# Kernel optimization log

Measured on AMD Instinct MI355X. Metric: run time of the kernel, lower is better.

## Reference

```python
import jax, jax.numpy as jnp
import numpy as np

B, N, IN_F, OUT_F, H, NUM_EDGE_TYPES = 16, 512, 256, 256, 8, 50
HEAD_DIM = OUT_F // H
LN_EPS = 1e-5


def setup_inputs() -> dict:
    key = jax.random.key(0)
    ks = jax.random.split(key, 8)
    x = jax.random.normal(ks[0], (B, N, IN_F), dtype=jnp.float32)
    adj = jax.random.randint(ks[1], (B, N, N), 0, 2, dtype=jnp.int32)
    edge_types = jax.random.randint(ks[2], (B, N, N), 0, NUM_EDGE_TYPES, dtype=jnp.int32)
    # Parameters (torch Linear stores weight as [out, in]; we keep [in, out] for x @ W)
    W = jax.random.normal(ks[3], (IN_F, OUT_F), dtype=jnp.float32) / np.sqrt(IN_F)
    a1 = jax.random.normal(ks[4], (HEAD_DIM,), dtype=jnp.float32) / np.sqrt(HEAD_DIM)
    a2 = jax.random.normal(ks[5], (HEAD_DIM,), dtype=jnp.float32) / np.sqrt(HEAD_DIM)
    edge_emb = jax.random.normal(ks[6], (NUM_EDGE_TYPES, H), dtype=jnp.float32) * 0.02
    edge_emb = edge_emb.at[0].set(0.0)  # padding_idx=0
    ln_gamma = jnp.ones((OUT_F,), dtype=jnp.float32)
    ln_beta = jnp.zeros((OUT_F,), dtype=jnp.float32)
    return {"x": x, "adj": adj, "edge_types": edge_types, "W": W, "a1": a1,
            "a2": a2, "edge_emb": edge_emb, "ln_gamma": ln_gamma, "ln_beta": ln_beta}


def reference(x, adj, edge_types, W, a1, a2, edge_emb, ln_gamma, ln_beta):
    Bx, Nx, _ = x.shape
    # Wh: [B, N, H, D]
    Wh = (x @ W).reshape(Bx, Nx, H, HEAD_DIM)
    # per-node attention scalars: [B, N, H]
    s1 = jnp.einsum('bnhd,d->bnh', Wh, a1)
    s2 = jnp.einsum('bnhd,d->bnh', Wh, a2)
    # e: [B, N(i), N(j), H]
    e = s1[:, :, None, :] + s2[:, None, :, :] + edge_emb[edge_types]
    e = jnp.where(e > 0, e, 0.2 * e)  # leaky_relu(0.2)
    e = jnp.where((adj == 0)[..., None], jnp.float32(-1e9), e)
    alpha = jax.nn.softmax(e, axis=2)  # softmax over j
    # (dropout omitted: eval mode / deterministic reference)
    h = jnp.einsum('bijh,bjhd->bihd', alpha, Wh).reshape(Bx, Nx, OUT_F)
    # LayerNorm over last dim
    mu = jnp.mean(h, axis=-1, keepdims=True)
    var = jnp.mean(jnp.square(h - mu), axis=-1, keepdims=True)
    hn = (h - mu) * jax.lax.rsqrt(var + LN_EPS) * ln_gamma + ln_beta
    return jax.nn.elu(hn)
```

## Files before the change

kernel.cpp:

```cpp
#include <hip/hip_runtime.h>
#include <hip/hip_bf16.h>
#include <stdint.h>

namespace gat {
constexpr int NB   = 16;
constexpr int NN   = 512;
constexpr int FIN  = 256;
constexpr int FOUT = 256;
constexpr int H    = 8;
constexpr int NE   = 50;
constexpr float L2E  = 1.4426950408889634f;
constexpr float MASK = -115.41500f;
}
using namespace gat;

typedef __attribute__((ext_vector_type(8))) short short8;
typedef __attribute__((ext_vector_type(4))) float f32x4;

__device__ __forceinline__ unsigned pk_bf16(unsigned ulo, unsigned uhi) {
  return __builtin_amdgcn_perm(uhi, ulo, 0x07060302u);
}
__device__ __forceinline__ unsigned pk2f(float a, float b) {
  return pk_bf16(__float_as_uint(a) + 0x8000u, __float_as_uint(b) + 0x8000u);
}

__global__ __launch_bounds__(256) void k_prep(const float* __restrict__ Wm,
                                              unsigned short* __restrict__ WbT) {
  const int k = blockIdx.x;
  const int f = threadIdx.x;
  const unsigned u = __float_as_uint(Wm[k * FOUT + f]) + 0x8000u;
  WbT[f * FIN + k] = (unsigned short)(u >> 16);
}

__global__ __launch_bounds__(256) void k_pack(const int* __restrict__ adj,
                                              const int* __restrict__ ety,
                                              unsigned* __restrict__ codes) {
  const size_t base = ((size_t)blockIdx.x * 256 + threadIdx.x) * 16;
  const int4* ap = (const int4*)(adj + base);
  const int4* ep = (const int4*)(ety + base);
  unsigned o[4];
  #pragma unroll
  for (int g = 0; g < 4; ++g) {
    const int4 a = ap[g];
    const int4 e = ep[g];
    o[g] = (unsigned)(e.x | (a.x << 6))
         | ((unsigned)(e.y | (a.y << 6)) << 8)
         | ((unsigned)(e.z | (a.z << 6)) << 16)
         | ((unsigned)(e.w | (a.w << 6)) << 24);
  }
  uint4 v; v.x = o[0]; v.y = o[1]; v.z = o[2]; v.w = o[3];
  *(uint4*)(codes + base / 4) = v;
}

__global__ __launch_bounds__(512, 4) void k_gemm(
    const float* __restrict__ x, const unsigned short* __restrict__ WbT,
    const float* __restrict__ a1, const float* __restrict__ a2,
    unsigned short* __restrict__ WhT, float* __restrict__ s1, float* __restrict__ s2T)
{
  __shared__ alignas(16) unsigned short xS[16 * 264];
  __shared__ float redG[256 * 18];
  const int t    = threadIdx.x;
  const int row0 = blockIdx.x * 16;

  {
    const int r  = t >> 5;
    const int kb = (t & 31) * 8;
    const float4* xg = (const float4*)(x + (size_t)(row0 + r) * FIN + kb);
    const float4 v0 = xg[0], v1 = xg[1];
    uint4 o;
    o.x = pk2f(v0.x, v0.y); o.y = pk2f(v0.z, v0.w);
    o.z = pk2f(v1.x, v1.y); o.w = pk2f(v1.z, v1.w);
    *(uint4*)&xS[r * 264 + kb] = o;
  }
  __syncthreads();

  const int W    = t >> 6;
  const int w    = W & 3;
  const int kh   = W >> 2;
  const int L    = t & 63;
  const int nn   = L & 15;
  const int quad = L >> 4;
  const unsigned short* wb = WbT + (size_t)(w * 64 + nn) * FIN + kh * 128 + quad * 8;
  const unsigned short* xp = &xS[nn * 264 + kh * 128 + quad * 8];

  f32x4 acc0 = {0.f,0.f,0.f,0.f}, acc1 = {0.f,0.f,0.f,0.f};
  f32x4 acc2 = {0.f,0.f,0.f,0.f}, acc3 = {0.f,0.f,0.f,0.f};

  #pragma unroll
  for (int kc = 0; kc < 4; ++kc) {
    const int k0 = kc * 32;
    const short8 A  = *(const short8*)(xp + k0);
    const short8 B0 = *(const short8*)(wb + k0);
    const short8 B1 = *(const short8*)(wb + 16 * FIN + k0);
    const short8 B2 = *(const short8*)(wb + 32 * FIN + k0);
    const short8 B3 = *(const short8*)(wb + 48 * FIN + k0);
    acc0 = __builtin_amdgcn_mfma_f32_16x16x32_bf16(A, B0, acc0, 0, 0, 0);
    acc1 = __builtin_amdgcn_mfma_f32_16x16x32_bf16(A, B1, acc1, 0, 0, 0);
    acc2 = __builtin_amdgcn_mfma_f32_16x16x32_bf16(A, B2, acc2, 0, 0, 0);
    acc3 = __builtin_amdgcn_mfma_f32_16x16x32_bf16(A, B3, acc3, 0, 0, 0);
  }

  const int tt = (w << 6) | L;
  if (kh == 1) {
    float* rp = redG + tt * 18;
    rp[0]=acc0[0]; rp[1]=acc0[1]; rp[2]=acc0[2]; rp[3]=acc0[3];
    rp[4]=acc1[0]; rp[5]=acc1[1]; rp[6]=acc1[2]; rp[7]=acc1[3];
    rp[8]=acc2[0]; rp[9]=acc2[1]; rp[10]=acc2[2]; rp[11]=acc2[3];
    rp[12]=acc3[0]; rp[13]=acc3[1]; rp[14]=acc3[2]; rp[15]=acc3[3];
  }
  __syncthreads();
  if (kh == 1) return;

  {
    const float* rp = redG + tt * 18;
    acc0[0]+=rp[0]; acc0[1]+=rp[1]; acc0[2]+=rp[2]; acc0[3]+=rp[3];
    acc1[0]+=rp[4]; acc1[1]+=rp[5]; acc1[2]+=rp[6]; acc1[3]+=rp[7];
    acc2[0]+=rp[8]; acc2[1]+=rp[9]; acc2[2]+=rp[10]; acc2[3]+=rp[11];
    acc3[0]+=rp[12]; acc3[1]+=rp[13]; acc3[2]+=rp[14]; acc3[3]+=rp[15];
  }

  const int b     = row0 >> 9;
  const int node0 = (row0 & 511) + quad * 4;
  f32x4 accs[4] = {acc0, acc1, acc2, acc3};

  #pragma unroll
  for (int ft = 0; ft < 4; ++ft) {
    const int f = w * 64 + ft * 16 + nn;
    uint2 o;
    o.x = pk2f(accs[ft][0], accs[ft][1]);
    o.y = pk2f(accs[ft][2], accs[ft][3]);
    *(uint2*)(WhT + (size_t)((b * 8 + (f >> 5)) * 32 + (f & 31)) * 512 + node0) = o;
  }

  const float a1lo = a1[nn], a1hi = a1[16 + nn];
  const float a2lo = a2[nn], a2hi = a2[16 + nn];
  #pragma unroll
  for (int hh = 0; hh < 2; ++hh) {
    const int h = w * 2 + hh;
    const f32x4 e0 = accs[hh * 2], e1 = accs[hh * 2 + 1];
    float p1[4], p2[4];
    #pragma unroll
    for (int r = 0; r < 4; ++r) {
      p1[r] = e0[r] * a1lo + e1[r] * a1hi;
      p2[r] = e0[r] * a2lo + e1[r] * a2hi;
    }
    #pragma unroll
    for (int r = 0; r < 4; ++r) {
      p1[r] += __shfl_xor(p1[r], 1); p2[r] += __shfl_xor(p2[r], 1);
      p1[r] += __shfl_xor(p1[r], 2); p2[r] += __shfl_xor(p2[r], 2);
      p1[r] += __shfl_xor(p1[r], 4); p2[r] += __shfl_xor(p2[r], 4);
      p1[r] += __shfl_xor(p1[r], 8); p2[r] += __shfl_xor(p2[r], 8);
    }
    if (nn == 0) {
      float4 sv; sv.x = p2[0] * L2E; sv.y = p2[1] * L2E; sv.z = p2[2] * L2E; sv.w = p2[3] * L2E;
      *(float4*)(s2T + (size_t)(b * 8 + h) * 512 + node0) = sv;
      #pragma unroll
      for (int r = 0; r < 4; ++r)
        s1[(size_t)(row0 + quad * 4 + r) * H + h] = p1[r] * L2E;
    }
  }
}

__global__ __launch_bounds__(512, 4) void k_attn(
    const unsigned char* __restrict__ codes,
    const float* __restrict__ s1, const float* __restrict__ s2T,
    const unsigned short* __restrict__ WhT, const float* __restrict__ emb,
    const float* __restrict__ gam, const float* __restrict__ bet,
    float* __restrict__ out)
{
  __shared__ float2 embS[4 * 64];
  __shared__ float2 lnS[16 * 4];
  __shared__ float  s2S[8 * 512];
  __shared__ float  redS[256 * 18];

  const int t    = threadIdx.x;
  const int b    = blockIdx.x >> 5;
  const int i0   = (blockIdx.x & 31) * 16;
  const int W    = t >> 6;
  const int w    = W & 3;
  const int jh   = W >> 2;
  const int L    = t & 63;
  const int i    = L & 15;
  const int quad = L >> 4;
  const int h0   = w, h1 = w + 4;

  {
    const float4* sg = (const float4*)(s2T + (size_t)b * 8 * 512);
    float4* ss = (float4*)s2S;
    ss[t]       = sg[t];
    ss[t + 512] = sg[t + 512];
  }
  if (t < 256) {
    const int wp = t >> 6, e = t & 63;
    if (e < NE) {
      float2 v; v.x = emb[e * H + wp] * L2E; v.y = emb[e * H + wp + 4] * L2E;
      embS[t] = v;
    }
  }

  const int row   = b * NN + i0 + i;
  const int jbase = jh * 256;

  uint2 cw[8];
  {
    const unsigned char* cp = codes + (size_t)row * NN + jbase + quad * 8;
    #pragma unroll
    for (int kc = 0; kc < 8; ++kc) cw[kc] = *(const uint2*)(cp + kc * 32);
  }

  const float si0 = s1[(size_t)row * H + h0];
  const float si1 = s1[(size_t)row * H + h1];
  const unsigned short* wt00 = WhT + (size_t)((b * 8 + h0) * 32 + i)      * 512;
  const unsigned short* wt01 = WhT + (size_t)((b * 8 + h0) * 32 + 16 + i) * 512;
  const unsigned short* wt10 = WhT + (size_t)((b * 8 + h1) * 32 + i)      * 512;
  const unsigned short* wt11 = WhT + (size_t)((b * 8 + h1) * 32 + 16 + i) * 512;

  f32x4 acc00 = {0.f,0.f,0.f,0.f}, acc01 = {0.f,0.f,0.f,0.f};
  f32x4 acc10 = {0.f,0.f,0.f,0.f}, acc11 = {0.f,0.f,0.f,0.f};
  float l0 = 0.f, l1 = 0.f;

  __syncthreads();

  #pragma unroll 2
  for (int kc = 0; kc < 8; ++kc) {
    const int ja = jbase + kc * 32 + quad * 8;
    const short8 A00 = *(const short8*)(wt00 + ja);
    const short8 A01 = *(const short8*)(wt01 + ja);
    const short8 A10 = *(const short8*)(wt10 + ja);
    const short8 A11 = *(const short8*)(wt11 + ja);
    const float4 sa0 = *(const float4*)&s2S[h0 * 512 + ja];
    const float4 sb0 = *(const float4*)&s2S[h0 * 512 + ja + 4];
    const float4 sa1 = *(const float4*)&s2S[h1 * 512 + ja];
    const float4 sb1 = *(const float4*)&s2S[h1 * 512 + ja + 4];

    const float s20[8] = {sa0.x, sa0.y, sa0.z, sa0.w, sb0.x, sb0.y, sb0.z, sb0.w};
    const float s21[8] = {sa1.x, sa1.y, sa1.z, sa1.w, sb1.x, sb1.y, sb1.z, sb1.w};

    unsigned u0[8], u1[8];
    #pragma unroll
    for (int q = 0; q < 8; ++q) {
      const unsigned cword = (q < 4) ? cw[kc].x : cw[kc].y;
      const unsigned c = (cword >> ((q & 3) * 8)) & 0x7fu;
      const bool on = c >= 64u;
      const float2 em = embS[w * 64 + (c & 63u)];
      float e0 = si0 + s20[q] + em.x;
      float e1 = si1 + s21[q] + em.y;
      e0 = fmaxf(e0, 0.2f * e0);
      e1 = fmaxf(e1, 0.2f * e1);
      e0 = on ? e0 : MASK;
      e1 = on ? e1 : MASK;
      const float p0 = exp2f(e0);
      const float p1 = exp2f(e1);
      l0 += p0; l1 += p1;
      u0[q] = __float_as_uint(p0) + 0x8000u;
      u1[q] = __float_as_uint(p1) + 0x8000u;
    }
    uint4 U0, U1;
    U0.x = pk_bf16(u0[0], u0[1]); U0.y = pk_bf16(u0[2], u0[3]);
    U0.z = pk_bf16(u0[4], u0[5]); U0.w = pk_bf16(u0[6], u0[7]);
    U1.x = pk_bf16(u1[0], u1[1]); U1.y = pk_bf16(u1[2], u1[3]);
    U1.z = pk_bf16(u1[4], u1[5]); U1.w = pk_bf16(u1[6], u1[7]);
    const short8 B0 = __builtin_bit_cast(short8, U0);
    const short8 B1 = __builtin_bit_cast(short8, U1);

    acc00 = __builtin_amdgcn_mfma_f32_16x16x32_bf16(A00, B0, acc00, 0, 0, 0);
    acc01 = __builtin_amdgcn_mfma_f32_16x16x32_bf16(A01, B0, acc01, 0, 0, 0);
    acc10 = __builtin_amdgcn_mfma_f32_16x16x32_bf16(A10, B1, acc10, 0, 0, 0);
    acc11 = __builtin_amdgcn_mfma_f32_16x16x32_bf16(A11, B1, acc11, 0, 0, 0);
  }

  l0 += __shfl_xor(l0, 16); l0 += __shfl_xor(l0, 32);
  l1 += __shfl_xor(l1, 16); l1 += __shfl_xor(l1, 32);

  const int tt = (w << 6) | L;
  if (jh == 1) {
    float* rp = redS + tt * 18;
    rp[0]=acc00[0]; rp[1]=acc00[1]; rp[2]=acc00[2]; rp[3]=acc00[3];
    rp[4]=acc01[0]; rp[5]=acc01[1]; rp[6]=acc01[2]; rp[7]=acc01[3];
    rp[8]=acc10[0]; rp[9]=acc10[1]; rp[10]=acc10[2]; rp[11]=acc10[3];
    rp[12]=acc11[0]; rp[13]=acc11[1]; rp[14]=acc11[2]; rp[15]=acc11[3];
    rp[16]=l0; rp[17]=l1;
  }
  __syncthreads();

  float vals[16]; float mu, rstd;
  if (jh == 0) {
    const float* rp = redS + tt * 18;
    acc00[0]+=rp[0]; acc00[1]+=rp[1]; acc00[2]+=rp[2]; acc00[3]+=rp[3];
    acc01[0]+=rp[4]; acc01[1]+=rp[5]; acc01[2]+=rp[6]; acc01[3]+=rp[7];
    acc10[0]+=rp[8]; acc10[1]+=rp[9]; acc10[2]+=rp[10]; acc10[3]+=rp[11];
    acc11[0]+=rp[12]; acc11[1]+=rp[13]; acc11[2]+=rp[14]; acc11[3]+=rp[15];
    l0 += rp[16]; l1 += rp[17];
    const float inv0 = __builtin_amdgcn_rcpf(l0);
    const float inv1 = __builtin_amdgcn_rcpf(l1);
    #pragma unroll
    for (int r = 0; r < 4; ++r) {
      vals[r]      = acc00[r] * inv0;
      vals[4 + r]  = acc01[r] * inv0;
      vals[8 + r]  = acc10[r] * inv1;
      vals[12 + r] = acc11[r] * inv1;
    }
    float s = 0.f, ss = 0.f;
    #pragma unroll
    for (int k = 0; k < 16; ++k) { s += vals[k]; ss += vals[k] * vals[k]; }
    s += __shfl_xor(s, 16); ss += __shfl_xor(ss, 16);
    s += __shfl_xor(s, 32); ss += __shfl_xor(ss, 32);
    if (quad == 0) { float2 v; v.x = s; v.y = ss; lnS[i * 4 + w] = v; }
  }
  __syncthreads();
  if (jh == 1) return;

  {
    float S = 0.f, SS = 0.f;
    #pragma unroll
    for (int ww = 0; ww < 4; ++ww) { const float2 v = lnS[i * 4 + ww]; S += v.x; SS += v.y; }
    mu = S * (1.0f / 256.0f);
    const float var = SS * (1.0f / 256.0f) - mu * mu;
    rstd = rsqrtf(var + 1e-5f);
  }

  const int fb[4] = { h0 * 32 + quad * 4, h0 * 32 + 16 + quad * 4,
                      h1 * 32 + quad * 4, h1 * 32 + 16 + quad * 4 };
  #pragma unroll
  for (int g = 0; g < 4; ++g) {
    const float4 gv = *(const float4*)(gam + fb[g]);
    const float4 bv = *(const float4*)(bet + fb[g]);
    float4 o;
    o.x = (vals[g*4+0] - mu) * rstd * gv.x + bv.x;
    o.y = (vals[g*4+1] - mu) * rstd * gv.y + bv.y;
    o.z = (vals[g*4+2] - mu) * rstd * gv.z + bv.z;
    o.w = (vals[g*4+3] - mu) * rstd * gv.w + bv.w;
    o.x = o.x > 0.f ? o.x : exp2f(o.x * L2E) - 1.f;
    o.y = o.y > 0.f ? o.y : exp2f(o.y * L2E) - 1.f;
    o.z = o.z > 0.f ? o.z : exp2f(o.z * L2E) - 1.f;
    o.w = o.w > 0.f ? o.w : exp2f(o.w * L2E) - 1.f;
    *(float4*)(out + (size_t)row * FOUT + fb[g]) = o;
  }
}

extern "C" void kernel_launch(void* const* d_in, const int* in_sizes, int n_in,
                              void* d_out, int out_size, void* d_ws, size_t ws_size,
                              hipStream_t stream) {
  (void)in_sizes; (void)n_in; (void)out_size; (void)ws_size;
  const float* x   = (const float*)d_in[0];
  const int*   adj = (const int*)  d_in[1];
  const int*   ety = (const int*)  d_in[2];
  const float* Wm  = (const float*)d_in[3];
  const float* a1  = (const float*)d_in[4];
  const float* a2  = (const float*)d_in[5];
  const float* emb = (const float*)d_in[6];
  const float* gam = (const float*)d_in[7];
  const float* bet = (const float*)d_in[8];
  float* out = (float*)d_out;

  unsigned short* WhT = (unsigned short*)d_ws;
  unsigned short* WbT = WhT + (size_t)NB * H * 32 * 512;
  float* s1   = (float*)(WbT + (size_t)FOUT * FIN);
  float* s2T  = s1 + (size_t)NB * NN * H;
  unsigned char* codes = (unsigned char*)(s2T + (size_t)NB * H * NN);

  k_prep<<<dim3(FIN),  dim3(256), 0, stream>>>(Wm, WbT);
  k_pack<<<dim3(NB * NN * NN / (256 * 16)), dim3(256), 0, stream>>>(adj, ety, (unsigned*)codes);
  k_gemm<<<dim3(NB * NN / 16), dim3(512), 0, stream>>>(x, WbT, a1, a2, WhT, s1, s2T);
  k_attn<<<dim3(NB * (NN / 16)), dim3(512), 0, stream>>>(codes, s1, s2T, WhT, emb, gam, bet, out);
}
```

Before: 138.6 us.

## Fold attention vectors into GEMM weights, merge prep kernels, prefetch WhT in attn

Merges the W transpose and adj/edge-type packing into a single preprocessing launch, and precomputes W·a1 and W·a2 per head as 16 extra bf16 weight columns. The GEMM then produces s1 and s2 with one extra MFMA in one wave, replacing the shuffle reductions and the split-K LDS reduction; it now uses 256 threads and covers the full K range per wave. The attention kernel stores s1 transposed, fully unrolls its loop and software-prefetches the next WhT fragments. This saves one launch and some GEMM epilogue work, but the scores are now computed from bf16-rounded folded weights, which changes numerics slightly.

```diff
diff --git a/kernel.cpp b/kernel.cpp
--- a/kernel.cpp
+++ b/kernel.cpp
@@ -23,71 +23,93 @@
 __device__ __forceinline__ unsigned pk2f(float a, float b) {
   return pk_bf16(__float_as_uint(a) + 0x8000u, __float_as_uint(b) + 0x8000u);
 }
-
-__global__ __launch_bounds__(256) void k_prep(const float* __restrict__ Wm,
-                                              unsigned short* __restrict__ WbT) {
-  const int k = blockIdx.x;
-  const int f = threadIdx.x;
-  const unsigned u = __float_as_uint(Wm[k * FOUT + f]) + 0x8000u;
-  WbT[f * FIN + k] = (unsigned short)(u >> 16);
-}
-
-__global__ __launch_bounds__(256) void k_pack(const int* __restrict__ adj,
-                                              const int* __restrict__ ety,
-                                              unsigned* __restrict__ codes) {
-  const size_t base = ((size_t)blockIdx.x * 256 + threadIdx.x) * 16;
-  const int4* ap = (const int4*)(adj + base);
-  const int4* ep = (const int4*)(ety + base);
-  unsigned o[4];
-  #pragma unroll
-  for (int g = 0; g < 4; ++g) {
-    const int4 a = ap[g];
-    const int4 e = ep[g];
-    o[g] = (unsigned)(e.x | (a.x << 6))
-         | ((unsigned)(e.y | (a.y << 6)) << 8)
-         | ((unsigned)(e.z | (a.z << 6)) << 16)
-         | ((unsigned)(e.w | (a.w << 6)) << 24);
-  }
-  uint4 v; v.x = o[0]; v.y = o[1]; v.z = o[2]; v.w = o[3];
-  *(uint4*)(codes + base / 4) = v;
-}
-
-__global__ __launch_bounds__(512, 4) void k_gemm(
-    const float* __restrict__ x, const unsigned short* __restrict__ WbT,
-    const float* __restrict__ a1, const float* __restrict__ a2,
-    unsigned short* __restrict__ WhT, float* __restrict__ s1, float* __restrict__ s2T)
+__device__ __forceinline__ unsigned short bf1(float a) {
+  return (unsigned short)((__float_as_uint(a) + 0x8000u) >> 16);
+}
+
+__global__ __launch_bounds__(256) void k_pre(const int* __restrict__ adj,
+                                             const int* __restrict__ ety,
+                                             const float* __restrict__ Wm,
+                                             const float* __restrict__ a1,
+                                             const float* __restrict__ a2,
+                                             unsigned* __restrict__ codes,
+                                             unsigned short* __restrict__ WbTa) {
+  const int blk = blockIdx.x;
+  if (blk < 1024) {
+    const size_t base = ((size_t)blk * 256 + threadIdx.x) * 16;
+    const int4* ap = (const int4*)(adj + base);
+    const int4* ep = (const int4*)(ety + base);
+    unsigned o[4];
+    #pragma unroll
+    for (int g = 0; g < 4; ++g) {
+      const int4 a = ap[g];
+      const int4 e = ep[g];
+      o[g] = (unsigned)(e.x | (a.x << 6))
+           | ((unsigned)(e.y | (a.y << 6)) << 8)
+           | ((unsigned)(e.z | (a.z << 6)) << 16)
+           | ((unsigned)(e.w | (a.w << 6)) << 24);
+    }
+    uint4 v; v.x = o[0]; v.y = o[1]; v.z = o[2]; v.w = o[3];
+    *(uint4*)(codes + base / 4) = v;
+  } else if (blk < 1280) {
+    const int k = blk - 1024;
+    const int f = threadIdx.x;
+    WbTa[f * FIN + k] = bf1(Wm[k * FOUT + f]);
+  } else {
+    const int k = threadIdx.x;
+    const float* wr = Wm + (size_t)k * FOUT;
+    #pragma unroll
+    for (int h = 0; h < H; ++h) {
+      float v1 = 0.f, v2 = 0.f;
+      #pragma unroll
+      for (int d = 0; d < 32; ++d) {
+        const float wv = wr[h * 32 + d];
+        v1 += wv * a1[d];
+        v2 += wv * a2[d];
+      }
+      WbTa[(256 + h) * FIN + k] = bf1(v1);
+      WbTa[(264 + h) * FIN + k] = bf1(v2);
+    }
+  }
+}
+
+__global__ __launch_bounds__(256, 4) void k_gemm(
+    const float* __restrict__ x, const unsigned short* __restrict__ WbTa,
+    unsigned short* __restrict__ WhT, float* __restrict__ s1T, float* __restrict__ s2T)
 {
   __shared__ alignas(16) unsigned short xS[16 * 264];
-  __shared__ float redG[256 * 18];
   const int t    = threadIdx.x;
   const int row0 = blockIdx.x * 16;
 
   {
-    const int r  = t >> 5;
-    const int kb = (t & 31) * 8;
+    const int r  = t >> 4;
+    const int kb = (t & 15) * 16;
     const float4* xg = (const float4*)(x + (size_t)(row0 + r) * FIN + kb);
-    const float4 v0 = xg[0], v1 = xg[1];
-    uint4 o;
-    o.x = pk2f(v0.x, v0.y); o.y = pk2f(v0.z, v0.w);
-    o.z = pk2f(v1.x, v1.y); o.w = pk2f(v1.z, v1.w);
-    *(uint4*)&xS[r * 264 + kb] = o;
+    const float4 v0 = xg[0], v1 = xg[1], v2 = xg[2], v3 = xg[3];
+    uint4 o0, o1;
+    o0.x = pk2f(v0.x, v0.y); o0.y = pk2f(v0.z, v0.w);
+    o0.z = pk2f(v1.x, v1.y); o0.w = pk2f(v1.z, v1.w);
+    o1.x = pk2f(v2.x, v2.y); o1.y = pk2f(v2.z, v2.w);
+    o1.z = pk2f(v3.x, v3.y); o1.w = pk2f(v3.z, v3.w);
+    *(uint4*)&xS[r * 264 + kb]     = o0;
+    *(uint4*)&xS[r * 264 + kb + 8] = o1;
   }
   __syncthreads();
 
-  const int W    = t >> 6;
-  const int w    = W & 3;
-  const int kh   = W >> 2;
+  const int w    = t >> 6;
   const int L    = t & 63;
   const int nn   = L & 15;
   const int quad = L >> 4;
-  const unsigned short* wb = WbT + (size_t)(w * 64 + nn) * FIN + kh * 128 + quad * 8;
-  const unsigned short* xp = &xS[nn * 264 + kh * 128 + quad * 8];
+  const unsigned short* wb = WbTa + (size_t)(w * 64 + nn) * FIN + quad * 8;
+  const unsigned short* wa = WbTa + (size_t)(256 + nn) * FIN + quad * 8;
+  const unsigned short* xp = &xS[nn * 264 + quad * 8];
 
   f32x4 acc0 = {0.f,0.f,0.f,0.f}, acc1 = {0.f,0.f,0.f,0.f};
   f32x4 acc2 = {0.f,0.f,0.f,0.f}, acc3 = {0.f,0.f,0.f,0.f};
+  f32x4 accA = {0.f,0.f,0.f,0.f};
 
   #pragma unroll
-  for (int kc = 0; kc < 4; ++kc) {
+  for (int kc = 0; kc < 8; ++kc) {
     const int k0 = kc * 32;
     const short8 A  = *(const short8*)(xp + k0);
     const short8 B0 = *(const short8*)(wb + k0);
@@ -98,25 +120,10 @@
     acc1 = __builtin_amdgcn_mfma_f32_16x16x32_bf16(A, B1, acc1, 0, 0, 0);
     acc2 = __builtin_amdgcn_mfma_f32_16x16x32_bf16(A, B2, acc2, 0, 0, 0);
     acc3 = __builtin_amdgcn_mfma_f32_16x16x32_bf16(A, B3, acc3, 0, 0, 0);
-  }
-
-  const int tt = (w << 6) | L;
-  if (kh == 1) {
-    float* rp = redG + tt * 18;
-    rp[0]=acc0[0]; rp[1]=acc0[1]; rp[2]=acc0[2]; rp[3]=acc0[3];
-    rp[4]=acc1[0]; rp[5]=acc1[1]; rp[6]=acc1[2]; rp[7]=acc1[3];
-    rp[8]=acc2[0]; rp[9]=acc2[1]; rp[10]=acc2[2]; rp[11]=acc2[3];
-    rp[12]=acc3[0]; rp[13]=acc3[1]; rp[14]=acc3[2]; rp[15]=acc3[3];
-  }
-  __syncthreads();
-  if (kh == 1) return;
-
-  {
-    const float* rp = redG + tt * 18;
-    acc0[0]+=rp[0]; acc0[1]+=rp[1]; acc0[2]+=rp[2]; acc0[3]+=rp[3];
-    acc1[0]+=rp[4]; acc1[1]+=rp[5]; acc1[2]+=rp[6]; acc1[3]+=rp[7];
-    acc2[0]+=rp[8]; acc2[1]+=rp[9]; acc2[2]+=rp[10]; acc2[3]+=rp[11];
-    acc3[0]+=rp[12]; acc3[1]+=rp[13]; acc3[2]+=rp[14]; acc3[3]+=rp[15];
+    if (w == 3) {
+      const short8 BA = *(const short8*)(wa + k0);
+      accA = __builtin_amdgcn_mfma_f32_16x16x32_bf16(A, BA, accA, 0, 0, 0);
+    }
   }
 
   const int b     = row0 >> 9;
@@ -132,38 +139,19 @@
     *(uint2*)(WhT + (size_t)((b * 8 + (f >> 5)) * 32 + (f & 31)) * 512 + node0) = o;
   }
 
-  const float a1lo = a1[nn], a1hi = a1[16 + nn];
-  const float a2lo = a2[nn], a2hi = a2[16 + nn];
-  #pragma unroll
-  for (int hh = 0; hh < 2; ++hh) {
-    const int h = w * 2 + hh;
-    const f32x4 e0 = accs[hh * 2], e1 = accs[hh * 2 + 1];
-    float p1[4], p2[4];
-    #pragma unroll
-    for (int r = 0; r < 4; ++r) {
-      p1[r] = e0[r] * a1lo + e1[r] * a1hi;
-      p2[r] = e0[r] * a2lo + e1[r] * a2hi;
-    }
-    #pragma unroll
-    for (int r = 0; r < 4; ++r) {
-      p1[r] += __shfl_xor(p1[r], 1); p2[r] += __shfl_xor(p2[r], 1);
-      p1[r] += __shfl_xor(p1[r], 2); p2[r] += __shfl_xor(p2[r], 2);
-      p1[r] += __shfl_xor(p1[r], 4); p2[r] += __shfl_xor(p2[r], 4);
-      p1[r] += __shfl_xor(p1[r], 8); p2[r] += __shfl_xor(p2[r], 8);
-    }
-    if (nn == 0) {
-      float4 sv; sv.x = p2[0] * L2E; sv.y = p2[1] * L2E; sv.z = p2[2] * L2E; sv.w = p2[3] * L2E;
-      *(float4*)(s2T + (size_t)(b * 8 + h) * 512 + node0) = sv;
-      #pragma unroll
-      for (int r = 0; r < 4; ++r)
-        s1[(size_t)(row0 + quad * 4 + r) * H + h] = p1[r] * L2E;
-    }
+  if (w == 3) {
+    float4 sv;
+    sv.x = accA[0] * L2E; sv.y = accA[1] * L2E;
+    sv.z = accA[2] * L2E; sv.w = accA[3] * L2E;
+    float* dst = (nn < 8) ? (s1T + (size_t)(b * 8 + nn) * 512 + node0)
+                          : (s2T + (size_t)(b * 8 + (nn - 8)) * 512 + node0);
+    *(float4*)dst = sv;
   }
 }
 
 __global__ __launch_bounds__(512, 4) void k_attn(
     const unsigned char* __restrict__ codes,
-    const float* __restrict__ s1, const float* __restrict__ s2T,
+    const float* __restrict__ s1T, const float* __restrict__ s2T,
     const unsigned short* __restrict__ WhT, const float* __restrict__ emb,
     const float* __restrict__ gam, const float* __restrict__ bet,
     float* __restrict__ out)
@@ -208,8 +196,8 @@
     for (int kc = 0; kc < 8; ++kc) cw[kc] = *(const uint2*)(cp + kc * 32);
   }
 
-  const float si0 = s1[(size_t)row * H + h0];
-  const float si1 = s1[(size_t)row * H + h1];
+  const float si0 = s1T[(size_t)(b * 8 + h0) * 512 + i0 + i];
+  const float si1 = s1T[(size_t)(b * 8 + h1) * 512 + i0 + i];
   const unsigned short* wt00 = WhT + (size_t)((b * 8 + h0) * 32 + i)      * 512;
   const unsigned short* wt01 = WhT + (size_t)((b * 8 + h0) * 32 + 16 + i) * 512;
   const unsigned short* wt10 = WhT + (size_t)((b * 8 + h1) * 32 + i)      * 512;
@@ -219,15 +207,25 @@
   f32x4 acc10 = {0.f,0.f,0.f,0.f}, acc11 = {0.f,0.f,0.f,0.f};
   float l0 = 0.f, l1 = 0.f;
 
+  const int ja0 = jbase + quad * 8;
+  short8 nA00 = *(const short8*)(wt00 + ja0);
+  short8 nA01 = *(const short8*)(wt01 + ja0);
+  short8 nA10 = *(const short8*)(wt10 + ja0);
+  short8 nA11 = *(const short8*)(wt11 + ja0);
+
   __syncthreads();
 
-  #pragma unroll 2
+  #pragma unroll
   for (int kc = 0; kc < 8; ++kc) {
-    const int ja = jbase + kc * 32 + quad * 8;
-    const short8 A00 = *(const short8*)(wt00 + ja);
-    const short8 A01 = *(const short8*)(wt01 + ja);
-    const short8 A10 = *(const short8*)(wt10 + ja);
-    const short8 A11 = *(const short8*)(wt11 + ja);
+    const int ja  = jbase + kc * 32 + quad * 8;
+    const short8 A00 = nA00, A01 = nA01, A10 = nA10, A11 = nA11;
+    {
+      const int jn = ja + 32;
+      nA00 = *(const short8*)(wt00 + jn);
+      nA01 = *(const short8*)(wt01 + jn);
+      nA10 = *(const short8*)(wt10 + jn);
+      nA11 = *(const short8*)(wt11 + jn);
+    }
     const float4 sa0 = *(const float4*)&s2S[h0 * 512 + ja];
     const float4 sb0 = *(const float4*)&s2S[h0 * 512 + ja + 4];
     const float4 sa1 = *(const float4*)&s2S[h1 * 512 + ja];
@@ -353,14 +351,13 @@
   const float* bet = (const float*)d_in[8];
   float* out = (float*)d_out;
 
-  unsigned short* WhT = (unsigned short*)d_ws;
-  unsigned short* WbT = WhT + (size_t)NB * H * 32 * 512;
-  float* s1   = (float*)(WbT + (size_t)FOUT * FIN);
-  float* s2T  = s1 + (size_t)NB * NN * H;
+  unsigned short* WhT  = (unsigned short*)d_ws;
+  unsigned short* WbTa = WhT + (size_t)NB * H * 32 * 512;
+  float* s1T  = (float*)(WbTa + (size_t)272 * FIN);
+  float* s2T  = s1T + (size_t)NB * H * NN;
   unsigned char* codes = (unsigned char*)(s2T + (size_t)NB * H * NN);
 
-  k_prep<<<dim3(FIN),  dim3(256), 0, stream>>>(Wm, WbT);
-  k_pack<<<dim3(NB * NN * NN / (256 * 16)), dim3(256), 0, stream>>>(adj, ety, (unsigned*)codes);
-  k_gemm<<<dim3(NB * NN / 16), dim3(512), 0, stream>>>(x, WbT, a1, a2, WhT, s1, s2T);
-  k_attn<<<dim3(NB * (NN / 16)), dim3(512), 0, stream>>>(codes, s1, s2T, WhT, emb, gam, bet, out);
-}
+  k_pre<<<dim3(1281), dim3(256), 0, stream>>>(adj, ety, Wm, a1, a2, (unsigned*)codes, WbTa);
+  k_gemm<<<dim3(NB * NN / 16), dim3(256), 0, stream>>>(x, WbTa, WhT, s1T, s2T);
+  k_attn<<<dim3(NB * (NN / 16)), dim3(512), 0, stream>>>(codes, s1T, s2T, WhT, emb, gam, bet, out);
+}
```

Result: no change. 136.8 us (-1.3%).
